# Performance work log

Hardware: AMD Instinct MI355X
Metric: run time of the kernel (lower is better)

## Reference

```python
import jax, jax.numpy as jnp
import numpy as np

N_QUBITS = 4
N_FEATURES = 16
B = 1048576


def _bcast(theta):
    # theta: scalar or [B]; make broadcastable against [B,2,2,2] amp slices
    return theta if jnp.ndim(theta) == 0 else theta.reshape(theta.shape[0], 1, 1, 1)


def apply_ry(state, theta, w):
    # state: [B,2,2,2,2] complex; RY(theta) on wire w
    th = _bcast(theta)
    c = jnp.cos(th / 2).astype(state.dtype)
    s = jnp.sin(th / 2).astype(state.dtype)
    st = jnp.moveaxis(state, w + 1, -1)
    a0, a1 = st[..., 0], st[..., 1]
    st = jnp.stack([c * a0 - s * a1, s * a0 + c * a1], axis=-1)
    return jnp.moveaxis(st, -1, w + 1)


def apply_rz(state, theta, w):
    # RZ(theta) = diag(e^{-i theta/2}, e^{+i theta/2}) on wire w
    th = _bcast(theta)
    ph = jnp.exp(-0.5j * th.astype(jnp.float32)).astype(state.dtype)
    st = jnp.moveaxis(state, w + 1, -1)
    a0, a1 = st[..., 0], st[..., 1]
    st = jnp.stack([ph * a0, jnp.conj(ph) * a1], axis=-1)
    return jnp.moveaxis(st, -1, w + 1)


def cnot(state, c, t):
    st = jnp.moveaxis(state, (c + 1, t + 1), (-2, -1))  # [...,2(ctrl),2(tgt)]
    st = jnp.stack([st[..., 0, :], st[..., 1, ::-1]], axis=-2)
    return jnp.moveaxis(st, (-2, -1), (c + 1, t + 1))


def quantum_encoder_batched(x, qw):
    # x: [B,16] float32, qw: [8] float32 -> latents [B,4] (PauliZ expvals)
    b = x.shape[0]
    state = jnp.zeros((b, 16), jnp.complex64).at[:, 0].set(1.0)
    state = state.reshape(b, 2, 2, 2, 2)
    pi = jnp.float32(np.pi)
    for i in range(N_QUBITS):
        state = apply_ry(state, x[:, i] * pi, i)
        state = apply_rz(state, x[:, i + N_QUBITS] * pi, i)
    for i in range(N_QUBITS - 1):
        state = cnot(state, i, i + 1)
    for i in range(N_QUBITS):
        state = apply_ry(state, qw[2 * i], i)
        state = apply_rz(state, qw[2 * i + 1], i)
    for i in range(N_QUBITS - 1):
        state = cnot(state, i, i + 1)
    probs = state.real ** 2 + state.imag ** 2  # [B,2,2,2,2]
    zs = []
    for i in range(N_QUBITS):
        axes = tuple(a for a in range(1, N_QUBITS + 1) if a != i + 1)
        p = probs.sum(axes)  # [B,2]
        zs.append(p[:, 0] - p[:, 1])
    return jnp.stack(zs, axis=1)  # [B,4]


def setup_inputs() -> dict:
    key = jax.random.key(0)
    ks = jax.random.split(key, 8)
    x = jax.random.uniform(ks[0], (B, N_FEATURES), dtype=jnp.float32)
    q_weights = 0.01 * jax.random.normal(ks[1], (2 * N_QUBITS,), dtype=jnp.float32)
    # decoder: Linear(4,16) -> ReLU -> Linear(16,32) -> ReLU -> Linear(32,16)
    W1 = jax.random.normal(ks[2], (16, 4), dtype=jnp.float32) / jnp.sqrt(4.0)
    b1 = jnp.zeros((16,), jnp.float32)
    W2 = jax.random.normal(ks[3], (32, 16), dtype=jnp.float32) / jnp.sqrt(16.0)
    b2 = jnp.zeros((32,), jnp.float32)
    W3 = jax.random.normal(ks[4], (16, 32), dtype=jnp.float32) / jnp.sqrt(32.0)
    b3 = jnp.zeros((16,), jnp.float32)
    return {"x": x, "q_weights": q_weights, "W1": W1, "b1": b1,
            "W2": W2, "b2": b2, "W3": W3, "b3": b3}


def reference(x, q_weights, W1, b1, W2, b2, W3, b3):
    z = quantum_encoder_batched(x, q_weights)          # [B,4]
    h = jax.nn.relu(z @ W1.T + b1)                      # [B,16]
    h = jax.nn.relu(h @ W2.T + b2)                      # [B,32]
    return h @ W3.T + b3                                # [B,16]
```

## Files before the change

### kernel.cpp

```cpp
#include <hip/hip_runtime.h>

using u16 = unsigned short;
using u32 = unsigned int;
typedef float v2f   __attribute__((ext_vector_type(2)));
typedef float f32x4 __attribute__((ext_vector_type(4)));
typedef short s16x8 __attribute__((ext_vector_type(8)));

__device__ __forceinline__ float bf2f(u32 b) { return __uint_as_float(b << 16); }
__device__ __forceinline__ u32   f2bf(float f) {
    u32 u = __float_as_uint(f);
    return (u + 0x7FFFu + ((u >> 16) & 1u)) >> 16;
}
__device__ __forceinline__ v2f pkfma(v2f a, v2f b, v2f c) { return __builtin_elementwise_fma(a, b, c); }
__device__ __forceinline__ v2f s2v(float x) { return (v2f){x, x}; }

__global__ void __launch_bounds__(256) qae_fused(
    const float* __restrict__ x,  const float* __restrict__ qw,
    const float* __restrict__ W1, const float* __restrict__ b1,
    const float* __restrict__ W2, const float* __restrict__ b2,
    const float* __restrict__ W3, const float* __restrict__ b3,
    float* __restrict__ out, int n)
{
    int tid  = threadIdx.x;
    int b    = blockIdx.x * 256 + tid;
    int bc   = b < n ? b : n - 1;
    int lane = tid & 63;
    int quad = lane >> 4, col = lane & 15;
    int wbase = (tid >> 6) * 64;

    __shared__ union {
        u16 frag[8 * 512];
        struct { u16 Zb[256 * 4]; u16 H1[256 * 24]; u16 H2[256 * 36]; } m;
    } sh;

    const float4* xf = reinterpret_cast<const float4*>(x);
    float4 xa = xf[(size_t)bc * 4];
    float4 xc = xf[(size_t)bc * 4 + 1];

    #pragma unroll
    for (int e = 0; e < 16; ++e) {
        int t  = tid * 16 + e;
        int f  = t >> 9, idx = t & 511;
        int ln = idx >> 3, j = idx & 7;
        int nn = ln & 15, qd = ln >> 4, k = qd * 8 + j;
        int ff = f >> 1;
        float w = 0.f; bool valid = false;
        if      (ff == 0) { valid = (k < 4);  if (valid) w = W1[nn * 4 + k]; }
        else if (ff == 1) { valid = (k < 16); if (valid) w = W2[nn * 16 + k]; }
        else if (ff == 2) { valid = (k < 16); if (valid) w = W2[(16 + nn) * 16 + k]; }
        else              { valid = true;               w = W3[nn * 32 + k]; }
        u16 hb = (u16)f2bf(w);
        u16 lb = (u16)f2bf(w - bf2f(hb));
        sh.frag[t] = valid ? ((f & 1) ? lb : hb) : (u16)0;
    }

    const float INV4PI = 0.07957747154594767f;
    float qc[4], qs[4];
    #pragma unroll
    for (int w = 0; w < 4; ++w) {
        float a = qw[2 * w];
        qc[w] = __builtin_amdgcn_cosf(a * INV4PI);
        qs[w] = __builtin_amdgcn_sinf(a * INV4PI);
    }

    float th[4] = { xa.x, xa.y, xa.z, xa.w };
    float ph[4] = { xc.x, xc.y, xc.z, xc.w };
    float u0r[4], u0i[4], u1r[4], u1i[4];
    #pragma unroll
    for (int i = 0; i < 4; ++i) {
        float ct = __builtin_amdgcn_cosf(th[i] * 0.25f);
        float st = __builtin_amdgcn_sinf(th[i] * 0.25f);
        float cp = __builtin_amdgcn_cosf(ph[i] * 0.25f);
        float sp = __builtin_amdgcn_sinf(ph[i] * 0.25f);
        u0r[i] = ct * cp;  u0i[i] = -ct * sp;
        u1r[i] = st * cp;  u1i[i] = st * sp;
    }
    float p01r[4], p01i[4], p23r[4], p23i[4];
    #pragma unroll
    for (int a = 0; a < 2; ++a)
        #pragma unroll
        for (int c = 0; c < 2; ++c) {
            float arq = a ? u1r[0] : u0r[0], aiq = a ? u1i[0] : u0i[0];
            float brq = c ? u1r[1] : u0r[1], biq = c ? u1i[1] : u0i[1];
            p01r[a*2+c] = arq*brq - aiq*biq;
            p01i[a*2+c] = arq*biq + aiq*brq;
            float crq = a ? u1r[2] : u0r[2], ciq = a ? u1i[2] : u0i[2];
            float drq = c ? u1r[3] : u0r[3], diq = c ? u1i[3] : u0i[3];
            p23r[a*2+c] = crq*drq - ciq*diq;
            p23i[a*2+c] = crq*diq + ciq*drq;
        }
    v2f amp[16];
    #pragma unroll
    for (int i = 0; i < 16; ++i) {
        int q0=(i>>3)&1, q1=(i>>2)&1, q2=(i>>1)&1, q3=i&1;
        int g = (q0<<3) | ((q1^q0)<<2) | ((q2^q1)<<1) | (q3^q2);
        int hi = g >> 2, lo = g & 3;
        amp[i] = (v2f){ p01r[hi]*p23r[lo] - p01i[hi]*p23i[lo],
                        p01r[hi]*p23i[lo] + p01i[hi]*p23r[lo] };
    }
    #pragma unroll
    for (int w = 0; w < 4; ++w) {
        v2f vc = s2v(qc[w]), vs = s2v(qs[w]);
        int stride = 1 << (3 - w);
        #pragma unroll
        for (int m = 0; m < 16; ++m) {
            if (m & stride) continue;
            int i0 = m, i1 = m | stride;
            v2f a0 = amp[i0], a1 = amp[i1];
            amp[i0] = pkfma(vc, a0, -(vs * a1));
            amp[i1] = pkfma(vc, a1,  (vs * a0));
        }
    }
    float p[16];
    #pragma unroll
    for (int i = 0; i < 16; ++i) {
        int q0=(i>>3)&1, q1=(i>>2)&1, q2=(i>>1)&1, q3=i&1;
        int g = (q0<<3) | ((q1^q0)<<2) | ((q2^q1)<<1) | (q3^q2);
        v2f q = amp[g] * amp[g];
        p[i] = q.x + q.y;
    }
    float s2a[8], s4[4];
    #pragma unroll
    for (int j = 0; j < 8; ++j) s2a[j] = p[2*j] + p[2*j+1];
    #pragma unroll
    for (int j = 0; j < 4; ++j) s4[j] = s2a[2*j] + s2a[2*j+1];
    float zv[4];
    zv[0] = (s4[0] + s4[1]) - (s4[2] + s4[3]);
    zv[1] = (s4[0] - s4[1]) + (s4[2] - s4[3]);
    zv[2] = (s2a[0]-s2a[1]) + (s2a[2]-s2a[3]) + (s2a[4]-s2a[5]) + (s2a[6]-s2a[7]);
    zv[3] = (p[0]-p[1]) + (p[2]-p[3]) + (p[4]-p[5]) + (p[6]-p[7])
          + (p[8]-p[9]) + (p[10]-p[11]) + (p[12]-p[13]) + (p[14]-p[15]);

    __syncthreads();
    union U { uint4 u; s16x8 s; };
    s16x8 Bf[8];
    #pragma unroll
    for (int f = 0; f < 8; ++f) {
        U cv; cv.u = *reinterpret_cast<const uint4*>(&sh.frag[f * 512 + lane * 8]);
        Bf[f] = cv.s;
    }
    float b1v = b1[col], b2v0 = b2[col], b2v1 = b2[16 + col], b3v = b3[col];
    __syncthreads();

    u32 zlo = f2bf(zv[0]) | (f2bf(zv[1]) << 16);
    u32 zhi = f2bf(zv[2]) | (f2bf(zv[3]) << 16);
    *reinterpret_cast<uint2*>(&sh.m.Zb[tid * 4]) = make_uint2(zlo, zhi);
    __syncthreads();

    #pragma unroll
    for (int t = 0; t < 4; ++t) {
        int arow = wbase + t * 16 + col;
        U av; av.u = make_uint4(0, 0, 0, 0);
        if (quad == 0) {
            uint2 z = *reinterpret_cast<const uint2*>(&sh.m.Zb[arow * 4]);
            av.u.x = z.x; av.u.y = z.y;
        }
        f32x4 c = { b1v, b1v, b1v, b1v };
        c = __builtin_amdgcn_mfma_f32_16x16x32_bf16(av.s, Bf[1], c, 0, 0, 0);
        c = __builtin_amdgcn_mfma_f32_16x16x32_bf16(av.s, Bf[0], c, 0, 0, 0);
        #pragma unroll
        for (int r = 0; r < 4; ++r) {
            int row = wbase + t * 16 + quad * 4 + r;
            sh.m.H1[row * 24 + col] = (u16)f2bf(fmaxf(c[r], 0.f));
        }
    }
    __syncthreads();

    #pragma unroll
    for (int t = 0; t < 4; ++t) {
        int arow = wbase + t * 16 + col;
        U av; av.u = make_uint4(0, 0, 0, 0);
        if (quad < 2)
            av.u = *reinterpret_cast<const uint4*>(&sh.m.H1[arow * 24 + quad * 8]);
        #pragma unroll
        for (int nt = 0; nt < 2; ++nt) {
            float bv = nt ? b2v1 : b2v0;
            f32x4 c = { bv, bv, bv, bv };
            c = __builtin_amdgcn_mfma_f32_16x16x32_bf16(av.s, Bf[3 + 2*nt], c, 0, 0, 0);
            c = __builtin_amdgcn_mfma_f32_16x16x32_bf16(av.s, Bf[2 + 2*nt], c, 0, 0, 0);
            #pragma unroll
            for (int r = 0; r < 4; ++r) {
                int row = wbase + t * 16 + quad * 4 + r;
                sh.m.H2[row * 36 + nt * 16 + col] = (u16)f2bf(fmaxf(c[r], 0.f));
            }
        }
    }
    __syncthreads();

    #pragma unroll
    for (int t = 0; t < 4; ++t) {
        int arow = wbase + t * 16 + col;
        uint2 u0 = *reinterpret_cast<const uint2*>(&sh.m.H2[arow * 36 + quad * 8]);
        uint2 u1 = *reinterpret_cast<const uint2*>(&sh.m.H2[arow * 36 + quad * 8 + 4]);
        U av; av.u = make_uint4(u0.x, u0.y, u1.x, u1.y);
        f32x4 c = { b3v, b3v, b3v, b3v };
        c = __builtin_amdgcn_mfma_f32_16x16x32_bf16(av.s, Bf[7], c, 0, 0, 0);
        c = __builtin_amdgcn_mfma_f32_16x16x32_bf16(av.s, Bf[6], c, 0, 0, 0);
        int rowbase = blockIdx.x * 256 + wbase + t * 16 + quad * 4;
        #pragma unroll
        for (int r = 0; r < 4; ++r) {
            int grow = rowbase + r;
            if (grow < n) out[(size_t)grow * 16 + col] = c[r];
        }
    }
}

extern "C" void kernel_launch(void* const* d_in, const int* in_sizes, int n_in,
                              void* d_out, int out_size, void* d_ws, size_t ws_size,
                              hipStream_t stream) {
    const float* x  = (const float*)d_in[0];
    const float* qw = (const float*)d_in[1];
    const float* W1 = (const float*)d_in[2];
    const float* b1 = (const float*)d_in[3];
    const float* W2 = (const float*)d_in[4];
    const float* b2 = (const float*)d_in[5];
    const float* W3 = (const float*)d_in[6];
    const float* b3 = (const float*)d_in[7];
    float* out = (float*)d_out;

    int n = in_sizes[0] / 16;
    int blocks = (n + 255) / 256;
    qae_fused<<<blocks, 256, 0, stream>>>(x, qw, W1, b1, W2, b2, W3, b3, out, n);
}
```

Baseline: 149.0 us.

## Replace LDS staging with bpermute register shuffles and transposed MFMA layout

Removes all shared memory and __syncthreads from the decoder MLP. Weights now load directly into per-lane register fragments as the A operand, and activations become the B operand, exchanged between layers with ds_bpermute. The output becomes one float4 store per lane instead of scalar stores. This cuts LDS traffic and barriers but adds cross-lane permute instructions and per-thread weight loads, and the hi/lo weight split now truncates the high half instead of rounding it.

```diff
diff --git a/kernel.cpp b/kernel.cpp
--- a/kernel.cpp
+++ b/kernel.cpp
@@ -6,15 +6,28 @@
 typedef float f32x4 __attribute__((ext_vector_type(4)));
 typedef short s16x8 __attribute__((ext_vector_type(8)));
 
-__device__ __forceinline__ float bf2f(u32 b) { return __uint_as_float(b << 16); }
-__device__ __forceinline__ u32   f2bf(float f) {
-    u32 u = __float_as_uint(f);
-    return (u + 0x7FFFu + ((u >> 16) & 1u)) >> 16;
+union FragU { u32 d[4]; s16x8 s; };
+
+__device__ __forceinline__ u32 rne16(u32 u) { return (u + 0x7FFFu + ((u >> 16) & 1u)) >> 16; }
+__device__ __forceinline__ u32 pk_bf16(float a, float b) {
+    return rne16(__float_as_uint(a)) | (rne16(__float_as_uint(b)) << 16);
+}
+__device__ __forceinline__ void split2(float w0, float w1, u32& hi, u32& lo) {
+    u32 u0 = __float_as_uint(w0), u1 = __float_as_uint(w1);
+    hi = (u0 >> 16) | (u1 & 0xFFFF0000u);
+    float r0 = w0 - __uint_as_float(u0 & 0xFFFF0000u);
+    float r1 = w1 - __uint_as_float(u1 & 0xFFFF0000u);
+    lo = pk_bf16(r0, r1);
+}
+__device__ __forceinline__ u32 bp(int ib, u32 v) {
+    return (u32)__builtin_amdgcn_ds_bpermute(ib, (int)v);
 }
 __device__ __forceinline__ v2f pkfma(v2f a, v2f b, v2f c) { return __builtin_elementwise_fma(a, b, c); }
 __device__ __forceinline__ v2f s2v(float x) { return (v2f){x, x}; }
-
-__global__ void __launch_bounds__(256) qae_fused(
+__device__ __forceinline__ f32x4 tov(float4 v) { return (f32x4){v.x, v.y, v.z, v.w}; }
+#define MFMA16 __builtin_amdgcn_mfma_f32_16x16x32_bf16
+
+__global__ void __launch_bounds__(256) qae_bperm(
     const float* __restrict__ x,  const float* __restrict__ qw,
     const float* __restrict__ W1, const float* __restrict__ b1,
     const float* __restrict__ W2, const float* __restrict__ b2,
@@ -25,43 +38,12 @@
     int b    = blockIdx.x * 256 + tid;
     int bc   = b < n ? b : n - 1;
     int lane = tid & 63;
-    int quad = lane >> 4, col = lane & 15;
-    int wbase = (tid >> 6) * 64;
-
-    __shared__ union {
-        u16 frag[8 * 512];
-        struct { u16 Zb[256 * 4]; u16 H1[256 * 24]; u16 H2[256 * 36]; } m;
-    } sh;
+    int vn   = lane & 15, vq = lane >> 4;
+    int gbase = blockIdx.x * 256 + (tid - lane);
 
     const float4* xf = reinterpret_cast<const float4*>(x);
     float4 xa = xf[(size_t)bc * 4];
     float4 xc = xf[(size_t)bc * 4 + 1];
-
-    #pragma unroll
-    for (int e = 0; e < 16; ++e) {
-        int t  = tid * 16 + e;
-        int f  = t >> 9, idx = t & 511;
-        int ln = idx >> 3, j = idx & 7;
-        int nn = ln & 15, qd = ln >> 4, k = qd * 8 + j;
-        int ff = f >> 1;
-        float w = 0.f; bool valid = false;
-        if      (ff == 0) { valid = (k < 4);  if (valid) w = W1[nn * 4 + k]; }
-        else if (ff == 1) { valid = (k < 16); if (valid) w = W2[nn * 16 + k]; }
-        else if (ff == 2) { valid = (k < 16); if (valid) w = W2[(16 + nn) * 16 + k]; }
-        else              { valid = true;               w = W3[nn * 32 + k]; }
-        u16 hb = (u16)f2bf(w);
-        u16 lb = (u16)f2bf(w - bf2f(hb));
-        sh.frag[t] = valid ? ((f & 1) ? lb : hb) : (u16)0;
-    }
-
-    const float INV4PI = 0.07957747154594767f;
-    float qc[4], qs[4];
-    #pragma unroll
-    for (int w = 0; w < 4; ++w) {
-        float a = qw[2 * w];
-        qc[w] = __builtin_amdgcn_cosf(a * INV4PI);
-        qs[w] = __builtin_amdgcn_sinf(a * INV4PI);
-    }
 
     float th[4] = { xa.x, xa.y, xa.z, xa.w };
     float ph[4] = { xc.x, xc.y, xc.z, xc.w };
@@ -92,15 +74,18 @@
     v2f amp[16];
     #pragma unroll
     for (int i = 0; i < 16; ++i) {
-        int q0=(i>>3)&1, q1=(i>>2)&1, q2=(i>>1)&1, q3=i&1;
-        int g = (q0<<3) | ((q1^q0)<<2) | ((q2^q1)<<1) | (q3^q2);
+        int q0i=(i>>3)&1, q1i=(i>>2)&1, q2i=(i>>1)&1, q3i=i&1;
+        int g = (q0i<<3) | ((q1i^q0i)<<2) | ((q2i^q1i)<<1) | (q3i^q2i);
         int hi = g >> 2, lo = g & 3;
         amp[i] = (v2f){ p01r[hi]*p23r[lo] - p01i[hi]*p23i[lo],
                         p01r[hi]*p23i[lo] + p01i[hi]*p23r[lo] };
     }
+    const float INV4PI = 0.07957747154594767f;
     #pragma unroll
     for (int w = 0; w < 4; ++w) {
-        v2f vc = s2v(qc[w]), vs = s2v(qs[w]);
+        float a = qw[2 * w];
+        v2f vc = s2v(__builtin_amdgcn_cosf(a * INV4PI));
+        v2f vs = s2v(__builtin_amdgcn_sinf(a * INV4PI));
         int stride = 1 << (3 - w);
         #pragma unroll
         for (int m = 0; m < 16; ++m) {
@@ -114,8 +99,8 @@
     float p[16];
     #pragma unroll
     for (int i = 0; i < 16; ++i) {
-        int q0=(i>>3)&1, q1=(i>>2)&1, q2=(i>>1)&1, q3=i&1;
-        int g = (q0<<3) | ((q1^q0)<<2) | ((q2^q1)<<1) | (q3^q2);
+        int q0i=(i>>3)&1, q1i=(i>>2)&1, q2i=(i>>1)&1, q3i=i&1;
+        int g = (q0i<<3) | ((q1i^q0i)<<2) | ((q2i^q1i)<<1) | (q3i^q2i);
         v2f q = amp[g] * amp[g];
         p[i] = q.x + q.y;
     }
@@ -124,84 +109,92 @@
     for (int j = 0; j < 8; ++j) s2a[j] = p[2*j] + p[2*j+1];
     #pragma unroll
     for (int j = 0; j < 4; ++j) s4[j] = s2a[2*j] + s2a[2*j+1];
-    float zv[4];
-    zv[0] = (s4[0] + s4[1]) - (s4[2] + s4[3]);
-    zv[1] = (s4[0] - s4[1]) + (s4[2] - s4[3]);
-    zv[2] = (s2a[0]-s2a[1]) + (s2a[2]-s2a[3]) + (s2a[4]-s2a[5]) + (s2a[6]-s2a[7]);
-    zv[3] = (p[0]-p[1]) + (p[2]-p[3]) + (p[4]-p[5]) + (p[6]-p[7])
-          + (p[8]-p[9]) + (p[10]-p[11]) + (p[12]-p[13]) + (p[14]-p[15]);
-
-    __syncthreads();
-    union U { uint4 u; s16x8 s; };
-    s16x8 Bf[8];
-    #pragma unroll
-    for (int f = 0; f < 8; ++f) {
-        U cv; cv.u = *reinterpret_cast<const uint4*>(&sh.frag[f * 512 + lane * 8]);
-        Bf[f] = cv.s;
-    }
-    float b1v = b1[col], b2v0 = b2[col], b2v1 = b2[16 + col], b3v = b3[col];
-    __syncthreads();
-
-    u32 zlo = f2bf(zv[0]) | (f2bf(zv[1]) << 16);
-    u32 zhi = f2bf(zv[2]) | (f2bf(zv[3]) << 16);
-    *reinterpret_cast<uint2*>(&sh.m.Zb[tid * 4]) = make_uint2(zlo, zhi);
-    __syncthreads();
+    float zv0 = (s4[0] + s4[1]) - (s4[2] + s4[3]);
+    float zv1 = (s4[0] - s4[1]) + (s4[2] - s4[3]);
+    float zv2 = (s2a[0]-s2a[1]) + (s2a[2]-s2a[3]) + (s2a[4]-s2a[5]) + (s2a[6]-s2a[7]);
+    float zv3 = (p[0]-p[1]) + (p[2]-p[3]) + (p[4]-p[5]) + (p[6]-p[7])
+              + (p[8]-p[9]) + (p[10]-p[11]) + (p[12]-p[13]) + (p[14]-p[15]);
+
+    u32 zd0 = pk_bf16(zv0, zv1);
+    u32 zd1 = pk_bf16(zv2, zv3);
+
+    bool q0 = (vq == 0), qlt2 = (vq < 2);
+    FragU A1h, A1l;
+    {
+        float4 w = reinterpret_cast<const float4*>(W1)[vn];
+        u32 h0,l0,h1,l1; split2(w.x, w.y, h0, l0); split2(w.z, w.w, h1, l1);
+        A1h.d[0] = q0 ? h0 : 0; A1h.d[1] = q0 ? h1 : 0; A1h.d[2] = 0; A1h.d[3] = 0;
+        A1l.d[0] = q0 ? l0 : 0; A1l.d[1] = q0 ? l1 : 0; A1l.d[2] = 0; A1l.d[3] = 0;
+    }
+    FragU A2ah, A2al, A2bh, A2bl, A3h, A3l;
+    {
+        const float4* p0 = reinterpret_cast<const float4*>(W2 + vn * 16 + (vq & 1) * 8);
+        const float4* p1 = reinterpret_cast<const float4*>(W2 + (16 + vn) * 16 + (vq & 1) * 8);
+        float4 a0 = p0[0], a1 = p0[1], c0 = p1[0], c1 = p1[1];
+        u32 h, l;
+        split2(a0.x,a0.y,h,l); A2ah.d[0]=qlt2?h:0; A2al.d[0]=qlt2?l:0;
+        split2(a0.z,a0.w,h,l); A2ah.d[1]=qlt2?h:0; A2al.d[1]=qlt2?l:0;
+        split2(a1.x,a1.y,h,l); A2ah.d[2]=qlt2?h:0; A2al.d[2]=qlt2?l:0;
+        split2(a1.z,a1.w,h,l); A2ah.d[3]=qlt2?h:0; A2al.d[3]=qlt2?l:0;
+        split2(c0.x,c0.y,h,l); A2bh.d[0]=qlt2?h:0; A2bl.d[0]=qlt2?l:0;
+        split2(c0.z,c0.w,h,l); A2bh.d[1]=qlt2?h:0; A2bl.d[1]=qlt2?l:0;
+        split2(c1.x,c1.y,h,l); A2bh.d[2]=qlt2?h:0; A2bl.d[2]=qlt2?l:0;
+        split2(c1.z,c1.w,h,l); A2bh.d[3]=qlt2?h:0; A2bl.d[3]=qlt2?l:0;
+        const float4* p3 = reinterpret_cast<const float4*>(W3 + vn * 32 + vq * 8);
+        float4 e0 = p3[0], e1 = p3[1];
+        split2(e0.x,e0.y,h,l); A3h.d[0]=h; A3l.d[0]=l;
+        split2(e0.z,e0.w,h,l); A3h.d[1]=h; A3l.d[1]=l;
+        split2(e1.x,e1.y,h,l); A3h.d[2]=h; A3l.d[2]=l;
+        split2(e1.z,e1.w,h,l); A3h.d[3]=h; A3l.d[3]=l;
+    }
+    float4 c1b = reinterpret_cast<const float4*>(b1)[vq];
+    float4 c2b0 = reinterpret_cast<const float4*>(b2)[vq];
+    float4 c2b1 = reinterpret_cast<const float4*>(b2)[4 + vq];
+    float4 c3b = reinterpret_cast<const float4*>(b3)[vq];
+
+    int i2a = ((((2 * vq)    ) & 3) * 16 + vn) * 4;
+    int i2b = ((((2 * vq) + 1) & 3) * 16 + vn) * 4;
 
     #pragma unroll
     for (int t = 0; t < 4; ++t) {
-        int arow = wbase + t * 16 + col;
-        U av; av.u = make_uint4(0, 0, 0, 0);
-        if (quad == 0) {
-            uint2 z = *reinterpret_cast<const uint2*>(&sh.m.Zb[arow * 4]);
-            av.u.x = z.x; av.u.y = z.y;
-        }
-        f32x4 c = { b1v, b1v, b1v, b1v };
-        c = __builtin_amdgcn_mfma_f32_16x16x32_bf16(av.s, Bf[1], c, 0, 0, 0);
-        c = __builtin_amdgcn_mfma_f32_16x16x32_bf16(av.s, Bf[0], c, 0, 0, 0);
-        #pragma unroll
-        for (int r = 0; r < 4; ++r) {
-            int row = wbase + t * 16 + quad * 4 + r;
-            sh.m.H1[row * 24 + col] = (u16)f2bf(fmaxf(c[r], 0.f));
-        }
-    }
-    __syncthreads();
-
-    #pragma unroll
-    for (int t = 0; t < 4; ++t) {
-        int arow = wbase + t * 16 + col;
-        U av; av.u = make_uint4(0, 0, 0, 0);
-        if (quad < 2)
-            av.u = *reinterpret_cast<const uint4*>(&sh.m.H1[arow * 24 + quad * 8]);
-        #pragma unroll
-        for (int nt = 0; nt < 2; ++nt) {
-            float bv = nt ? b2v1 : b2v0;
-            f32x4 c = { bv, bv, bv, bv };
-            c = __builtin_amdgcn_mfma_f32_16x16x32_bf16(av.s, Bf[3 + 2*nt], c, 0, 0, 0);
-            c = __builtin_amdgcn_mfma_f32_16x16x32_bf16(av.s, Bf[2 + 2*nt], c, 0, 0, 0);
-            #pragma unroll
-            for (int r = 0; r < 4; ++r) {
-                int row = wbase + t * 16 + quad * 4 + r;
-                sh.m.H2[row * 36 + nt * 16 + col] = (u16)f2bf(fmaxf(c[r], 0.f));
-            }
-        }
-    }
-    __syncthreads();
-
-    #pragma unroll
-    for (int t = 0; t < 4; ++t) {
-        int arow = wbase + t * 16 + col;
-        uint2 u0 = *reinterpret_cast<const uint2*>(&sh.m.H2[arow * 36 + quad * 8]);
-        uint2 u1 = *reinterpret_cast<const uint2*>(&sh.m.H2[arow * 36 + quad * 8 + 4]);
-        U av; av.u = make_uint4(u0.x, u0.y, u1.x, u1.y);
-        f32x4 c = { b3v, b3v, b3v, b3v };
-        c = __builtin_amdgcn_mfma_f32_16x16x32_bf16(av.s, Bf[7], c, 0, 0, 0);
-        c = __builtin_amdgcn_mfma_f32_16x16x32_bf16(av.s, Bf[6], c, 0, 0, 0);
-        int rowbase = blockIdx.x * 256 + wbase + t * 16 + quad * 4;
-        #pragma unroll
-        for (int r = 0; r < 4; ++r) {
-            int grow = rowbase + r;
-            if (grow < n) out[(size_t)grow * 16 + col] = c[r];
-        }
+        int viL = (t * 16 + vn) * 4;
+        FragU B1; B1.d[0] = bp(viL, zd0); B1.d[1] = bp(viL, zd1); B1.d[2] = 0; B1.d[3] = 0;
+        f32x4 c1 = tov(c1b);
+        c1 = MFMA16(A1l.s, B1.s, c1, 0, 0, 0);
+        c1 = MFMA16(A1h.s, B1.s, c1, 0, 0, 0);
+        u32 da0 = pk_bf16(fmaxf(c1[0], 0.f), fmaxf(c1[1], 0.f));
+        u32 da1 = pk_bf16(fmaxf(c1[2], 0.f), fmaxf(c1[3], 0.f));
+
+        FragU B2;
+        B2.d[0] = bp(i2a, da0); B2.d[1] = bp(i2a, da1);
+        B2.d[2] = bp(i2b, da0); B2.d[3] = bp(i2b, da1);
+        f32x4 ca = tov(c2b0), cb = tov(c2b1);
+        ca = MFMA16(A2al.s, B2.s, ca, 0, 0, 0);
+        ca = MFMA16(A2ah.s, B2.s, ca, 0, 0, 0);
+        cb = MFMA16(A2bl.s, B2.s, cb, 0, 0, 0);
+        cb = MFMA16(A2bh.s, B2.s, cb, 0, 0, 0);
+        u32 ea0 = pk_bf16(fmaxf(ca[0],0.f), fmaxf(ca[1],0.f));
+        u32 ea1 = pk_bf16(fmaxf(ca[2],0.f), fmaxf(ca[3],0.f));
+        u32 eb0 = pk_bf16(fmaxf(cb[0],0.f), fmaxf(cb[1],0.f));
+        u32 eb1 = pk_bf16(fmaxf(cb[2],0.f), fmaxf(cb[3],0.f));
+
+        u32 s0a = bp(i2a, ea0), s0b = bp(i2a, eb0);
+        u32 s1a = bp(i2a, ea1), s1b = bp(i2a, eb1);
+        u32 s2_ = bp(i2b, ea0), s2b = bp(i2b, eb0);
+        u32 s3a = bp(i2b, ea1), s3b = bp(i2b, eb1);
+        FragU B3;
+        B3.d[0] = qlt2 ? s0a : s0b;
+        B3.d[1] = qlt2 ? s1a : s1b;
+        B3.d[2] = qlt2 ? s2_ : s2b;
+        B3.d[3] = qlt2 ? s3a : s3b;
+        f32x4 c3 = tov(c3b);
+        c3 = MFMA16(A3l.s, B3.s, c3, 0, 0, 0);
+        c3 = MFMA16(A3h.s, B3.s, c3, 0, 0, 0);
+
+        int R = gbase + t * 16 + vn;
+        if (R < n)
+            *reinterpret_cast<float4*>(out + (size_t)R * 16 + vq * 4) =
+                make_float4(c3[0], c3[1], c3[2], c3[3]);
     }
 }
 
@@ -220,5 +213,5 @@
 
     int n = in_sizes[0] / 16;
     int blocks = (n + 255) / 256;
-    qae_fused<<<blocks, 256, 0, stream>>>(x, qw, W1, b1, W2, b2, W3, b3, out, n);
-}
+    qae_bperm<<<blocks, 256, 0, stream>>>(x, qw, W1, b1, W2, b2, W3, b3, out, n);
+}
```

Result: faster. 135.0 us (-9.4%).
